# Optimization experiments

Measured on AMD Instinct MI355X. Metric: run time of the kernel, lower is better.

The kernel has to match this reference:

```python
import jax, jax.numpy as jnp
import numpy as np

B, T, C = 4, 2048, 1024
H = 16
D = C // H  # head_dim = 64


def setup_inputs() -> dict:
    key = jax.random.key(0)
    k1, k2, k3, k4, k5 = jax.random.split(key, 5)
    s = 0.02
    return {
        "x": jax.random.normal(k1, (B, T, C), dtype=jnp.float32),
        "W_qkv": jax.random.normal(k2, (C, 3 * C), dtype=jnp.float32) * s,
        "b_qkv": jax.random.normal(k3, (3 * C,), dtype=jnp.float32) * s,
        "W_o": jax.random.normal(k4, (C, C), dtype=jnp.float32) * s,
        "b_o": jax.random.normal(k5, (C,), dtype=jnp.float32) * s,
    }


def reference(x, W_qkv, b_qkv, W_o, b_o):
    b, t, c = x.shape
    scaling = D ** (-0.5)
    qkv = x @ W_qkv + b_qkv                      # [B,T,3C]
    q, k, v = jnp.split(qkv, 3, axis=-1)         # each [B,T,C]
    q = q.reshape(b, t, H, D).transpose(0, 2, 1, 3)  # [B,H,T,D]
    k = k.reshape(b, t, H, D).transpose(0, 2, 1, 3)
    v = v.reshape(b, t, H, D).transpose(0, 2, 1, 3)
    scores = jnp.einsum("bhqd,bhkd->bhqk", q, k) * scaling  # [B,H,T,T]
    mask = jnp.tril(jnp.ones((t, t), dtype=bool))            # causal
    scores = jnp.where(mask[None, None, :, :], scores, -jnp.inf)
    probs = jax.nn.softmax(scores, axis=-1)
    out = jnp.einsum("bhqk,bhkd->bhqd", probs, v)            # [B,H,T,D]
    out = out.transpose(0, 2, 1, 3).reshape(b, t, c)         # [B,T,C]
    return out @ W_o + b_o
```

## Files before the change

kernel.cpp:

```cpp
#include <hip/hip_runtime.h>
#include <hip/hip_bf16.h>

typedef unsigned short ushort_t;
typedef __attribute__((ext_vector_type(8))) short short8;
typedef __attribute__((ext_vector_type(4))) float floatx4;
typedef __attribute__((ext_vector_type(2))) unsigned uint2v;
typedef __attribute__((ext_vector_type(4))) unsigned uint4v;

#define B_ 4
#define T_ 2048
#define C_ 1024
#define H_ 16
#define D_ 64
#define BT_ (B_ * T_)
#define N3C (3 * C_)

#define KSC 0.18033688011112042f

__device__ __forceinline__ ushort_t f2bf(float f) {
    unsigned u = __float_as_uint(f);
    u += 0x7FFF + ((u >> 16) & 1);
    return (ushort_t)(u >> 16);
}
__device__ __forceinline__ unsigned pack2bf(float a, float b) {
    __hip_bfloat162 h = __float22bfloat162_rn(make_float2(a, b));
    return *(unsigned*)&h;
}

__device__ __forceinline__ void gload16(const ushort_t* g, ushort_t* l) {
    __builtin_amdgcn_global_load_lds((const __attribute__((address_space(1))) void*)g,
                                     (__attribute__((address_space(3))) void*)l, 16, 0, 0);
}

__global__ void prep_k(const float* __restrict__ x, ushort_t* __restrict__ xb,
                       const float* __restrict__ Wqkv, ushort_t* __restrict__ WqkvT,
                       const float* __restrict__ Wo, ushort_t* __restrict__ WoT) {
    __shared__ ushort_t t[32][33];
    int id = blockIdx.x;
    if (id < 4096) {
        size_t i = ((size_t)id * 256 + threadIdx.x) * 8;
        const float* xf = x + i;
        float4 a = *(const float4*)xf;
        float4 b = *(const float4*)(xf + 4);
        short8 o;
        o[0] = (short)f2bf(a.x); o[1] = (short)f2bf(a.y);
        o[2] = (short)f2bf(a.z); o[3] = (short)f2bf(a.w);
        o[4] = (short)f2bf(b.x); o[5] = (short)f2bf(b.y);
        o[6] = (short)f2bf(b.z); o[7] = (short)f2bf(b.w);
        *(short8*)&xb[i] = o;
        return;
    }
    int tt = id - 4096;
    int bx = tt & 127, by = tt >> 7;
    const float* in;
    ushort_t* out;
    int Nc, bc;
    if (bx < 96) { in = Wqkv; out = WqkvT; Nc = N3C; bc = bx * 32; }
    else         { in = Wo;   out = WoT;   Nc = C_;  bc = (bx - 96) * 32; }
    int br = by * 32;
    int lx = threadIdx.x & 31, ly = threadIdx.x >> 5;
#pragma unroll
    for (int i = 0; i < 4; ++i) {
        int r = ly + i * 8;
        t[r][lx] = f2bf(in[(size_t)(br + r) * Nc + bc + lx]);
    }
    __syncthreads();
#pragma unroll
    for (int i = 0; i < 4; ++i) {
        int r = ly + i * 8;
        out[(size_t)(bc + r) * C_ + br + lx] = t[lx][r];
    }
}

__global__ void vtrans_k(const ushort_t* __restrict__ in, ushort_t* __restrict__ out) {
    __shared__ ushort_t t[32][33];
    int bh = blockIdx.z;
    const ushort_t* I = in + (size_t)bh * T_ * D_;
    ushort_t* O = out + (size_t)bh * D_ * T_;
    int bt = blockIdx.x * 32, bd = blockIdx.y * 32;
    int lx = threadIdx.x & 31, ly = threadIdx.x >> 5;
#pragma unroll
    for (int i = 0; i < 4; ++i) {
        int r = ly + i * 8;
        t[r][lx] = I[(size_t)(bt + r) * D_ + bd + lx];
    }
    __syncthreads();
#pragma unroll
    for (int i = 0; i < 4; ++i) {
        int r = ly + i * 8;
        O[(size_t)(bd + r) * T_ + bt + lx] = t[lx][r];
    }
}

template <int MODE>
__launch_bounds__(256)
__global__ void gemm_bt(const ushort_t* __restrict__ A, const ushort_t* __restrict__ Bt,
                        const float* __restrict__ bias, float* __restrict__ Cout,
                        ushort_t* __restrict__ Qo, ushort_t* __restrict__ Ko,
                        ushort_t* __restrict__ Vo, int M, int N, int K) {
    __shared__ __align__(16) ushort_t Alds[2][128 * 32];
    __shared__ __align__(16) ushort_t Blds[2][128 * 32];
    int tid = threadIdx.x;
    int wave = tid >> 6, lane = tid & 63;
    int bm = blockIdx.x * 128, bn = blockIdx.y * 128;
    int wr = (wave >> 1) * 64, wc = (wave & 1) * 64;
    int lm = lane & 15, lk = (lane >> 4) * 8, lq = lane >> 4;

    floatx4 acc[4][4] = {};

    int srow = tid >> 2;
    int scol = (tid & 3) * 8;
    const ushort_t* Ab = A + (size_t)(bm + srow) * K + scol;
    const ushort_t* Bb = Bt + (size_t)(bn + srow) * K + scol;
    int lo0 = wave * 512, lo1 = 2048 + wave * 512;
    size_t rowskip = (size_t)64 * K;

    gload16(Ab, &Alds[0][lo0]);
    gload16(Ab + rowskip, &Alds[0][lo1]);
    gload16(Bb, &Blds[0][lo0]);
    gload16(Bb + rowskip, &Blds[0][lo1]);
    __syncthreads();

    int cur = 0;
    for (int k0 = 0; k0 < K; k0 += 32) {
        if (k0 + 32 < K) {
            gload16(Ab + k0 + 32, &Alds[cur ^ 1][lo0]);
            gload16(Ab + k0 + 32 + rowskip, &Alds[cur ^ 1][lo1]);
            gload16(Bb + k0 + 32, &Blds[cur ^ 1][lo0]);
            gload16(Bb + k0 + 32 + rowskip, &Blds[cur ^ 1][lo1]);
        }
        short8 af[4], bf[4];
#pragma unroll
        for (int i = 0; i < 4; ++i)
            af[i] = *(const short8*)&Alds[cur][(wr + i * 16 + lm) * 32 + lk];
#pragma unroll
        for (int i = 0; i < 4; ++i)
            bf[i] = *(const short8*)&Blds[cur][(wc + i * 16 + lm) * 32 + lk];
#pragma unroll
        for (int mi = 0; mi < 4; ++mi)
#pragma unroll
            for (int ni = 0; ni < 4; ++ni)
                acc[mi][ni] = __builtin_amdgcn_mfma_f32_16x16x32_bf16(
                    af[mi], bf[ni], acc[mi][ni], 0, 0, 0);
        __syncthreads();
        cur ^= 1;
    }

#pragma unroll
    for (int mi = 0; mi < 4; ++mi) {
#pragma unroll
        for (int ni = 0; ni < 4; ++ni) {
            int col = bn + wc + ni * 16 + lm;
            float bv = bias[col];
#pragma unroll
            for (int r = 0; r < 4; ++r) {
                int row = bm + wr + mi * 16 + lq * 4 + r;
                float v = acc[mi][ni][r] + bv;
                if (MODE == 0) {
                    Cout[(size_t)row * N + col] = v;
                } else {
                    int b = row >> 11, t = row & (T_ - 1);
                    int which = col >> 10, c = col & (C_ - 1);
                    int h = c >> 6, d = c & 63;
                    int bh = b * H_ + h;
                    size_t idx = ((size_t)bh * T_ + t) * D_ + d;
                    if (which == 0)
                        Qo[idx] = f2bf(v * KSC);
                    else if (which == 1)
                        Ko[idx] = f2bf(v);
                    else
                        Vo[idx] = f2bf(v);
                }
            }
        }
    }
}

__launch_bounds__(256)
__global__ void attn_k(const ushort_t* __restrict__ Q, const ushort_t* __restrict__ K,
                       const ushort_t* __restrict__ Vt, ushort_t* __restrict__ O) {
    __shared__ __align__(16) ushort_t KV[2][2][64 * 64];

    int tid = threadIdx.x, wave = tid >> 6, lane = tid & 63;
    int id = blockIdx.x;
    int xcd = id & 7, j = id >> 3;
    int band = 31 - (j & 31);
    int bh = xcd + 8 * (j >> 5);
    int b = bh >> 4, h = bh & 15;
    int lm = lane & 15, lq = lane >> 4, m7 = lane & 7;

    const ushort_t* Qp = Q + (size_t)bh * T_ * D_;
    const ushort_t* Kp = K + (size_t)bh * T_ * D_;
    const ushort_t* Vp = Vt + (size_t)bh * D_ * T_;
    ushort_t* Ob = O + ((size_t)b * T_) * C_ + h * D_;

    int sr = lane >> 3;
    int sc = (lane & 7) ^ sr;
    const ushort_t* Kst = Kp + (size_t)(wave * 16 + sr) * D_ + sc * 8;
    const ushort_t* Vst = Vp + (size_t)(wave * 16 + sr) * T_ + sc * 8;
    int lds0 = (wave * 2 + 0) * 512;
    int lds1 = (wave * 2 + 1) * 512;

    short8 onesf = {};
    if (lm == 0) {
#pragma unroll
        for (int jj = 0; jj < 8; ++jj) onesf[jj] = (short)0x3F80;
    }

    int m0 = band * 64 + wave * 16;

    short8 qf0 = *(const short8*)&Qp[(size_t)(m0 + lm) * D_ + lq * 8];
    short8 qf1 = *(const short8*)&Qp[(size_t)(m0 + lm) * D_ + 32 + lq * 8];

    floatx4 oacc[5] = {};

    int ntw = band + 1;

    gload16(Kst, &KV[0][0][lds0]);
    gload16(Kst + (size_t)8 * D_, &KV[0][0][lds1]);
    gload16(Vst, &KV[0][1][lds0]);
    gload16(Vst + (size_t)8 * T_, &KV[0][1][lds1]);
    __syncthreads();

    int cur = 0;
    for (int it = 0; it < ntw; ++it) {
        if (it + 1 < ntw) {
            size_t kv0n = (size_t)(it + 1) * 64;
            gload16(Kst + kv0n * D_, &KV[cur ^ 1][0][lds0]);
            gload16(Kst + kv0n * D_ + 8 * D_, &KV[cur ^ 1][0][lds1]);
            gload16(Vst + kv0n, &KV[cur ^ 1][1][lds0]);
            gload16(Vst + kv0n + 8 * T_, &KV[cur ^ 1][1][lds1]);
        }
        const ushort_t* Kb = &KV[cur][0][0];
        const ushort_t* Vb = &KV[cur][1][0];

        short8 kf[4][2], vf[4][2];
#pragma unroll
        for (int nt = 0; nt < 4; ++nt) {
            kf[nt][0] = *(const short8*)&Kb[(nt * 16 + lm) * 64 + ((lq ^ m7) * 8)];
            kf[nt][1] = *(const short8*)&Kb[(nt * 16 + lm) * 64 + (((lq + 4) ^ m7) * 8)];
        }

        floatx4 st[4] = {};
        __builtin_amdgcn_s_setprio(1);
#pragma unroll
        for (int nt = 0; nt < 4; ++nt) {
            st[nt] = __builtin_amdgcn_mfma_f32_16x16x32_bf16(kf[nt][0], qf0, st[nt], 0, 0, 0);
            st[nt] = __builtin_amdgcn_mfma_f32_16x16x32_bf16(kf[nt][1], qf1, st[nt], 0, 0, 0);
        }
        __builtin_amdgcn_s_setprio(0);

#pragma unroll
        for (int dt = 0; dt < 4; ++dt) {
            vf[dt][0] = *(const short8*)&Vb[(dt * 16 + lm) * 64 + ((lq ^ m7) * 8)];
            vf[dt][1] = *(const short8*)&Vb[(dt * 16 + lm) * 64 + (((lq + 4) ^ m7) * 8)];
        }

        int kv0 = it * 64;
        if (it == ntw - 1) {
            int mg = m0 + lm;
#pragma unroll
            for (int nt = 0; nt < 4; ++nt)
#pragma unroll
                for (int r = 0; r < 4; ++r) {
                    int kvg = kv0 + nt * 16 + lq * 4 + r;
                    if (kvg > mg) st[nt][r] = -__builtin_inff();
                }
        }

        unsigned e0 = pack2bf(__builtin_amdgcn_exp2f(st[0][0]), __builtin_amdgcn_exp2f(st[0][1]));
        unsigned e1 = pack2bf(__builtin_amdgcn_exp2f(st[0][2]), __builtin_amdgcn_exp2f(st[0][3]));
        unsigned e2 = pack2bf(__builtin_amdgcn_exp2f(st[1][0]), __builtin_amdgcn_exp2f(st[1][1]));
        unsigned e3 = pack2bf(__builtin_amdgcn_exp2f(st[1][2]), __builtin_amdgcn_exp2f(st[1][3]));
        unsigned e4 = pack2bf(__builtin_amdgcn_exp2f(st[2][0]), __builtin_amdgcn_exp2f(st[2][1]));
        unsigned e5 = pack2bf(__builtin_amdgcn_exp2f(st[2][2]), __builtin_amdgcn_exp2f(st[2][3]));
        unsigned e6 = pack2bf(__builtin_amdgcn_exp2f(st[3][0]), __builtin_amdgcn_exp2f(st[3][1]));
        unsigned e7 = pack2bf(__builtin_amdgcn_exp2f(st[3][2]), __builtin_amdgcn_exp2f(st[3][3]));

        uint2v ra = __builtin_amdgcn_permlane32_swap(e0, e2, false, false);
        uint2v wa = __builtin_amdgcn_permlane16_swap(ra[0], ra[1], false, false);
        uint2v rb = __builtin_amdgcn_permlane32_swap(e1, e3, false, false);
        uint2v wb = __builtin_amdgcn_permlane16_swap(rb[0], rb[1], false, false);
        uint2v rc = __builtin_amdgcn_permlane32_swap(e4, e6, false, false);
        uint2v wc = __builtin_amdgcn_permlane16_swap(rc[0], rc[1], false, false);
        uint2v rd = __builtin_amdgcn_permlane32_swap(e5, e7, false, false);
        uint2v wd = __builtin_amdgcn_permlane16_swap(rd[0], rd[1], false, false);

        short8 pb0 = __builtin_bit_cast(short8, (uint4v){wa[0], wb[0], wa[1], wb[1]});
        short8 pb1 = __builtin_bit_cast(short8, (uint4v){wc[0], wd[0], wc[1], wd[1]});

        __builtin_amdgcn_s_setprio(1);
#pragma unroll
        for (int dt = 0; dt < 4; ++dt) {
            oacc[dt] = __builtin_amdgcn_mfma_f32_16x16x32_bf16(vf[dt][0], pb0, oacc[dt], 0, 0, 0);
            oacc[dt] = __builtin_amdgcn_mfma_f32_16x16x32_bf16(vf[dt][1], pb1, oacc[dt], 0, 0, 0);
        }
        oacc[4] = __builtin_amdgcn_mfma_f32_16x16x32_bf16(onesf, pb0, oacc[4], 0, 0, 0);
        oacc[4] = __builtin_amdgcn_mfma_f32_16x16x32_bf16(onesf, pb1, oacc[4], 0, 0, 0);
        __builtin_amdgcn_s_setprio(0);

        __syncthreads();
        cur ^= 1;
    }

    float li = __shfl(oacc[4][0], lm, 64);
    float inv = 1.0f / li;
    int tg = m0 + lm;
#pragma unroll
    for (int dt = 0; dt < 4; ++dt) {
        uint2 pk;
        pk.x = pack2bf(oacc[dt][0] * inv, oacc[dt][1] * inv);
        pk.y = pack2bf(oacc[dt][2] * inv, oacc[dt][3] * inv);
        *(uint2*)&Ob[(size_t)tg * C_ + dt * 16 + lq * 4] = pk;
    }
}

extern "C" void kernel_launch(void* const* d_in, const int* in_sizes, int n_in,
                              void* d_out, int out_size, void* d_ws, size_t ws_size,
                              hipStream_t stream) {
    const float* x    = (const float*)d_in[0];
    const float* Wqkv = (const float*)d_in[1];
    const float* bqkv = (const float*)d_in[2];
    const float* Wo   = (const float*)d_in[3];
    const float* bo   = (const float*)d_in[4];

    ushort_t* ws = (ushort_t*)d_ws;
    ushort_t* WqkvT = ws;
    ushort_t* WoT   = WqkvT + (size_t)N3C * C_;
    ushort_t* Xb    = WoT + (size_t)C_ * C_;
    ushort_t* Qs    = Xb + (size_t)BT_ * C_;
    ushort_t* Ks    = Qs + (size_t)BT_ * C_;
    ushort_t* Vs    = Ks + (size_t)BT_ * C_;
    ushort_t* Attn  = Vs + (size_t)BT_ * C_;

    prep_k<<<8192, 256, 0, stream>>>(x, Xb, Wqkv, WqkvT, Wo, WoT);
    gemm_bt<1><<<dim3(BT_ / 128, N3C / 128), 256, 0, stream>>>(
        Xb, WqkvT, bqkv, nullptr, Qs, Ks, Attn, BT_, N3C, C_);
    vtrans_k<<<dim3(T_ / 32, D_ / 32, B_ * H_), 256, 0, stream>>>(Attn, Vs);
    attn_k<<<2048, 256, 0, stream>>>(Qs, Ks, Vs, Attn);
    gemm_bt<0><<<dim3(BT_ / 128, C_ / 128), 256, 0, stream>>>(
        Attn, WoT, bo, (float*)d_out, nullptr, nullptr, nullptr, BT_, C_, C_);
}
```

Measured before the change: 261.5 us.

## Restructure causal attention into 512-thread blocks with paired balanced query bands

The attention kernel now launches 512 blocks of 8 waves, each handling a 128-row query band. Each block processes two bands in sequence, pairing band 15-q with band q so every block does the same amount of causal work. K/V tiles of 64 rows are staged once per block and shared by all 8 waves, with each thread issuing one load per tile. The cost is that waves whose rows lie entirely before a KV tile sit idle at its barrier, and there are fewer, larger blocks.

```diff
diff --git a/kernel.cpp b/kernel.cpp
--- a/kernel.cpp
+++ b/kernel.cpp
@@ -176,7 +176,7 @@
     }
 }
 
-__launch_bounds__(256)
+__launch_bounds__(512)
 __global__ void attn_k(const ushort_t* __restrict__ Q, const ushort_t* __restrict__ K,
                        const ushort_t* __restrict__ Vt, ushort_t* __restrict__ O) {
     __shared__ __align__(16) ushort_t KV[2][2][64 * 64];
@@ -184,8 +184,8 @@
     int tid = threadIdx.x, wave = tid >> 6, lane = tid & 63;
     int id = blockIdx.x;
     int xcd = id & 7, j = id >> 3;
-    int band = 31 - (j & 31);
-    int bh = xcd + 8 * (j >> 5);
+    int q = j & 7, g = j >> 3;
+    int bh = xcd + 8 * g;
     int b = bh >> 4, h = bh & 15;
     int lm = lane & 15, lq = lane >> 4, m7 = lane & 7;
 
@@ -194,12 +194,11 @@
     const ushort_t* Vp = Vt + (size_t)bh * D_ * T_;
     ushort_t* Ob = O + ((size_t)b * T_) * C_ + h * D_;
 
-    int sr = lane >> 3;
-    int sc = (lane & 7) ^ sr;
-    const ushort_t* Kst = Kp + (size_t)(wave * 16 + sr) * D_ + sc * 8;
-    const ushort_t* Vst = Vp + (size_t)(wave * 16 + sr) * T_ + sc * 8;
-    int lds0 = (wave * 2 + 0) * 512;
-    int lds1 = (wave * 2 + 1) * 512;
+    int sr = tid >> 3;
+    int sc = (tid & 7) ^ (sr & 7);
+    const ushort_t* Kst = Kp + (size_t)sr * D_ + sc * 8;
+    const ushort_t* Vst = Vp + (size_t)sr * T_ + sc * 8;
+    int ldsb = wave * 512;
 
     short8 onesf = {};
     if (lm == 0) {
@@ -207,111 +206,112 @@
         for (int jj = 0; jj < 8; ++jj) onesf[jj] = (short)0x3F80;
     }
 
-    int m0 = band * 64 + wave * 16;
-
-    short8 qf0 = *(const short8*)&Qp[(size_t)(m0 + lm) * D_ + lq * 8];
-    short8 qf1 = *(const short8*)&Qp[(size_t)(m0 + lm) * D_ + 32 + lq * 8];
-
-    floatx4 oacc[5] = {};
-
-    int ntw = band + 1;
-
-    gload16(Kst, &KV[0][0][lds0]);
-    gload16(Kst + (size_t)8 * D_, &KV[0][0][lds1]);
-    gload16(Vst, &KV[0][1][lds0]);
-    gload16(Vst + (size_t)8 * T_, &KV[0][1][lds1]);
-    __syncthreads();
-
     int cur = 0;
-    for (int it = 0; it < ntw; ++it) {
-        if (it + 1 < ntw) {
-            size_t kv0n = (size_t)(it + 1) * 64;
-            gload16(Kst + kv0n * D_, &KV[cur ^ 1][0][lds0]);
-            gload16(Kst + kv0n * D_ + 8 * D_, &KV[cur ^ 1][0][lds1]);
-            gload16(Vst + kv0n, &KV[cur ^ 1][1][lds0]);
-            gload16(Vst + kv0n + 8 * T_, &KV[cur ^ 1][1][lds1]);
+#pragma unroll
+    for (int pass = 0; pass < 2; ++pass) {
+        int band = pass ? q : 15 - q;
+        int m0 = band * 128 + wave * 16;
+        int ntw = 2 * band + 2;
+
+        short8 qf0 = *(const short8*)&Qp[(size_t)(m0 + lm) * D_ + lq * 8];
+        short8 qf1 = *(const short8*)&Qp[(size_t)(m0 + lm) * D_ + 32 + lq * 8];
+
+        floatx4 oacc[5] = {};
+
+        gload16(Kst, &KV[cur][0][ldsb]);
+        gload16(Vst, &KV[cur][1][ldsb]);
+        __syncthreads();
+
+        for (int it = 0; it < ntw; ++it) {
+            if (it + 1 < ntw) {
+                size_t kv0n = (size_t)(it + 1) * 64;
+                gload16(Kst + kv0n * D_, &KV[cur ^ 1][0][ldsb]);
+                gload16(Vst + kv0n, &KV[cur ^ 1][1][ldsb]);
+            }
+            int kv0 = it * 64;
+            if (kv0 <= m0 + 15) {
+                const ushort_t* Kb = &KV[cur][0][0];
+                const ushort_t* Vb = &KV[cur][1][0];
+
+                short8 kf[4][2], vf[4][2];
+#pragma unroll
+                for (int nt = 0; nt < 4; ++nt) {
+                    kf[nt][0] = *(const short8*)&Kb[(nt * 16 + lm) * 64 + ((lq ^ m7) * 8)];
+                    kf[nt][1] = *(const short8*)&Kb[(nt * 16 + lm) * 64 + (((lq + 4) ^ m7) * 8)];
+                }
+
+                floatx4 st[4] = {};
+                __builtin_amdgcn_s_setprio(1);
+#pragma unroll
+                for (int nt = 0; nt < 4; ++nt) {
+                    st[nt] = __builtin_amdgcn_mfma_f32_16x16x32_bf16(kf[nt][0], qf0, st[nt], 0, 0, 0);
+                    st[nt] = __builtin_amdgcn_mfma_f32_16x16x32_bf16(kf[nt][1], qf1, st[nt], 0, 0, 0);
+                }
+                __builtin_amdgcn_s_setprio(0);
+
+#pragma unroll
+                for (int dt = 0; dt < 4; ++dt) {
+                    vf[dt][0] = *(const short8*)&Vb[(dt * 16 + lm) * 64 + ((lq ^ m7) * 8)];
+                    vf[dt][1] = *(const short8*)&Vb[(dt * 16 + lm) * 64 + (((lq + 4) ^ m7) * 8)];
+                }
+
+                if (kv0 + 63 > m0) {
+                    int mg = m0 + lm;
+#pragma unroll
+                    for (int nt = 0; nt < 4; ++nt)
+#pragma unroll
+                        for (int r = 0; r < 4; ++r) {
+                            int kvg = kv0 + nt * 16 + lq * 4 + r;
+                            if (kvg > mg) st[nt][r] = -__builtin_inff();
+                        }
+                }
+
+                unsigned e0 = pack2bf(__builtin_amdgcn_exp2f(st[0][0]), __builtin_amdgcn_exp2f(st[0][1]));
+                unsigned e1 = pack2bf(__builtin_amdgcn_exp2f(st[0][2]), __builtin_amdgcn_exp2f(st[0][3]));
+                unsigned e2 = pack2bf(__builtin_amdgcn_exp2f(st[1][0]), __builtin_amdgcn_exp2f(st[1][1]));
+                unsigned e3 = pack2bf(__builtin_amdgcn_exp2f(st[1][2]), __builtin_amdgcn_exp2f(st[1][3]));
+                unsigned e4 = pack2bf(__builtin_amdgcn_exp2f(st[2][0]), __builtin_amdgcn_exp2f(st[2][1]));
+                unsigned e5 = pack2bf(__builtin_amdgcn_exp2f(st[2][2]), __builtin_amdgcn_exp2f(st[2][3]));
+                unsigned e6 = pack2bf(__builtin_amdgcn_exp2f(st[3][0]), __builtin_amdgcn_exp2f(st[3][1]));
+                unsigned e7 = pack2bf(__builtin_amdgcn_exp2f(st[3][2]), __builtin_amdgcn_exp2f(st[3][3]));
+
+                uint2v ra = __builtin_amdgcn_permlane32_swap(e0, e2, false, false);
+                uint2v wa = __builtin_amdgcn_permlane16_swap(ra[0], ra[1], false, false);
+                uint2v rb = __builtin_amdgcn_permlane32_swap(e1, e3, false, false);
+                uint2v wb = __builtin_amdgcn_permlane16_swap(rb[0], rb[1], false, false);
+                uint2v rc = __builtin_amdgcn_permlane32_swap(e4, e6, false, false);
+                uint2v wc = __builtin_amdgcn_permlane16_swap(rc[0], rc[1], false, false);
+                uint2v rd = __builtin_amdgcn_permlane32_swap(e5, e7, false, false);
+                uint2v wd = __builtin_amdgcn_permlane16_swap(rd[0], rd[1], false, false);
+
+                short8 pb0 = __builtin_bit_cast(short8, (uint4v){wa[0], wb[0], wa[1], wb[1]});
+                short8 pb1 = __builtin_bit_cast(short8, (uint4v){wc[0], wd[0], wc[1], wd[1]});
+
+                __builtin_amdgcn_s_setprio(1);
+#pragma unroll
+                for (int dt = 0; dt < 4; ++dt) {
+                    oacc[dt] = __builtin_amdgcn_mfma_f32_16x16x32_bf16(vf[dt][0], pb0, oacc[dt], 0, 0, 0);
+                    oacc[dt] = __builtin_amdgcn_mfma_f32_16x16x32_bf16(vf[dt][1], pb1, oacc[dt], 0, 0, 0);
+                }
+                oacc[4] = __builtin_amdgcn_mfma_f32_16x16x32_bf16(onesf, pb0, oacc[4], 0, 0, 0);
+                oacc[4] = __builtin_amdgcn_mfma_f32_16x16x32_bf16(onesf, pb1, oacc[4], 0, 0, 0);
+                __builtin_amdgcn_s_setprio(0);
+            }
+
+            __syncthreads();
+            cur ^= 1;
         }
-        const ushort_t* Kb = &KV[cur][0][0];
-        const ushort_t* Vb = &KV[cur][1][0];
-
-        short8 kf[4][2], vf[4][2];
-#pragma unroll
-        for (int nt = 0; nt < 4; ++nt) {
-            kf[nt][0] = *(const short8*)&Kb[(nt * 16 + lm) * 64 + ((lq ^ m7) * 8)];
-            kf[nt][1] = *(const short8*)&Kb[(nt * 16 + lm) * 64 + (((lq + 4) ^ m7) * 8)];
+
+        float li = __shfl(oacc[4][0], lm, 64);
+        float inv = 1.0f / li;
+        int tg = m0 + lm;
+#pragma unroll
+        for (int dt = 0; dt < 4; ++dt) {
+            uint2 pk;
+            pk.x = pack2bf(oacc[dt][0] * inv, oacc[dt][1] * inv);
+            pk.y = pack2bf(oacc[dt][2] * inv, oacc[dt][3] * inv);
+            *(uint2*)&Ob[(size_t)tg * C_ + dt * 16 + lq * 4] = pk;
         }
-
-        floatx4 st[4] = {};
-        __builtin_amdgcn_s_setprio(1);
-#pragma unroll
-        for (int nt = 0; nt < 4; ++nt) {
-            st[nt] = __builtin_amdgcn_mfma_f32_16x16x32_bf16(kf[nt][0], qf0, st[nt], 0, 0, 0);
-            st[nt] = __builtin_amdgcn_mfma_f32_16x16x32_bf16(kf[nt][1], qf1, st[nt], 0, 0, 0);
-        }
-        __builtin_amdgcn_s_setprio(0);
-
-#pragma unroll
-        for (int dt = 0; dt < 4; ++dt) {
-            vf[dt][0] = *(const short8*)&Vb[(dt * 16 + lm) * 64 + ((lq ^ m7) * 8)];
-            vf[dt][1] = *(const short8*)&Vb[(dt * 16 + lm) * 64 + (((lq + 4) ^ m7) * 8)];
-        }
-
-        int kv0 = it * 64;
-        if (it == ntw - 1) {
-            int mg = m0 + lm;
-#pragma unroll
-            for (int nt = 0; nt < 4; ++nt)
-#pragma unroll
-                for (int r = 0; r < 4; ++r) {
-                    int kvg = kv0 + nt * 16 + lq * 4 + r;
-                    if (kvg > mg) st[nt][r] = -__builtin_inff();
-                }
-        }
-
-        unsigned e0 = pack2bf(__builtin_amdgcn_exp2f(st[0][0]), __builtin_amdgcn_exp2f(st[0][1]));
-        unsigned e1 = pack2bf(__builtin_amdgcn_exp2f(st[0][2]), __builtin_amdgcn_exp2f(st[0][3]));
-        unsigned e2 = pack2bf(__builtin_amdgcn_exp2f(st[1][0]), __builtin_amdgcn_exp2f(st[1][1]));
-        unsigned e3 = pack2bf(__builtin_amdgcn_exp2f(st[1][2]), __builtin_amdgcn_exp2f(st[1][3]));
-        unsigned e4 = pack2bf(__builtin_amdgcn_exp2f(st[2][0]), __builtin_amdgcn_exp2f(st[2][1]));
-        unsigned e5 = pack2bf(__builtin_amdgcn_exp2f(st[2][2]), __builtin_amdgcn_exp2f(st[2][3]));
-        unsigned e6 = pack2bf(__builtin_amdgcn_exp2f(st[3][0]), __builtin_amdgcn_exp2f(st[3][1]));
-        unsigned e7 = pack2bf(__builtin_amdgcn_exp2f(st[3][2]), __builtin_amdgcn_exp2f(st[3][3]));
-
-        uint2v ra = __builtin_amdgcn_permlane32_swap(e0, e2, false, false);
-        uint2v wa = __builtin_amdgcn_permlane16_swap(ra[0], ra[1], false, false);
-        uint2v rb = __builtin_amdgcn_permlane32_swap(e1, e3, false, false);
-        uint2v wb = __builtin_amdgcn_permlane16_swap(rb[0], rb[1], false, false);
-        uint2v rc = __builtin_amdgcn_permlane32_swap(e4, e6, false, false);
-        uint2v wc = __builtin_amdgcn_permlane16_swap(rc[0], rc[1], false, false);
-        uint2v rd = __builtin_amdgcn_permlane32_swap(e5, e7, false, false);
-        uint2v wd = __builtin_amdgcn_permlane16_swap(rd[0], rd[1], false, false);
-
-        short8 pb0 = __builtin_bit_cast(short8, (uint4v){wa[0], wb[0], wa[1], wb[1]});
-        short8 pb1 = __builtin_bit_cast(short8, (uint4v){wc[0], wd[0], wc[1], wd[1]});
-
-        __builtin_amdgcn_s_setprio(1);
-#pragma unroll
-        for (int dt = 0; dt < 4; ++dt) {
-            oacc[dt] = __builtin_amdgcn_mfma_f32_16x16x32_bf16(vf[dt][0], pb0, oacc[dt], 0, 0, 0);
-            oacc[dt] = __builtin_amdgcn_mfma_f32_16x16x32_bf16(vf[dt][1], pb1, oacc[dt], 0, 0, 0);
-        }
-        oacc[4] = __builtin_amdgcn_mfma_f32_16x16x32_bf16(onesf, pb0, oacc[4], 0, 0, 0);
-        oacc[4] = __builtin_amdgcn_mfma_f32_16x16x32_bf16(onesf, pb1, oacc[4], 0, 0, 0);
-        __builtin_amdgcn_s_setprio(0);
-
-        __syncthreads();
-        cur ^= 1;
-    }
-
-    float li = __shfl(oacc[4][0], lm, 64);
-    float inv = 1.0f / li;
-    int tg = m0 + lm;
-#pragma unroll
-    for (int dt = 0; dt < 4; ++dt) {
-        uint2 pk;
-        pk.x = pack2bf(oacc[dt][0] * inv, oacc[dt][1] * inv);
-        pk.y = pack2bf(oacc[dt][2] * inv, oacc[dt][3] * inv);
-        *(uint2*)&Ob[(size_t)tg * C_ + dt * 16 + lq * 4] = pk;
     }
 }
 
@@ -337,7 +337,7 @@
     gemm_bt<1><<<dim3(BT_ / 128, N3C / 128), 256, 0, stream>>>(
         Xb, WqkvT, bqkv, nullptr, Qs, Ks, Attn, BT_, N3C, C_);
     vtrans_k<<<dim3(T_ / 32, D_ / 32, B_ * H_), 256, 0, stream>>>(Attn, Vs);
-    attn_k<<<2048, 256, 0, stream>>>(Qs, Ks, Vs, Attn);
+    attn_k<<<512, 512, 0, stream>>>(Qs, Ks, Vs, Attn);
     gemm_bt<0><<<dim3(BT_ / 128, C_ / 128), 256, 0, stream>>>(
         Attn, WoT, bo, (float*)d_out, nullptr, nullptr, nullptr, BT_, C_, C_);
 }
```

Result: faster. 244.4 us (-6.5%).
